# Optimization experiments

Measured on AMD Instinct MI355X. Metric: run time of the kernel, lower is better.

## Reference

```python
import jax, jax.numpy as jnp
import numpy as np
from jax import lax

RF = 19       # receptive field: layers*(kernel-1)+1 = 3*6+1
WINDOW = 12
N_MIX = 2
K = 20        # subgraph_size (top-k per row)
GDEP = 2
ALPHA = 0.05  # propalpha
EPS = 1e-5


def conv2d(x, w, b):
    # x: [N,C,H,W], w: [O,I,1,k], valid conv along time (last) axis
    o = lax.conv_general_dilated(x, w, (1, 1), 'VALID',
                                 dimension_numbers=('NCHW', 'OIHW', 'NCHW'))
    return o + b[None, :, None, None]


def dilated_inception(x, ws, b):
    # ws: kernels [co, ci, k] for k in (2,3,6,7); dilation factor is 1 here
    outs = [lax.conv_general_dilated(x, w[:, :, None, :], (1, 1), 'VALID',
                                     dimension_numbers=('NCHW', 'OIHW', 'NCHW'))
            for w in ws]
    L = outs[-1].shape[-1]  # truncate to shortest (largest kernel) length
    out = jnp.concatenate([o[..., -L:] for o in outs], axis=1)
    return out + b[None, :, None, None]


def build_adj(e1, e2, l1w, l1b, l2w, l2b):
    # e1,e2: [M2,N,D] embedding tables (idx = arange -> full table)
    # torch Linear: y = x @ W.T + b, W: [out,in]
    nv1 = jnp.einsum('mnd,mod->mno', e1, l1w) + l1b[:, None, :]
    nv2 = jnp.einsum('mnd,mod->mno', e2, l2w) + l2b[:, None, :]
    a = jnp.einsum('mnd,mkd->mnk', nv1, nv2)  # [M2, N, N] per-block adjacency
    rows = [jnp.concatenate([a[i * N_MIX + j] for j in range(N_MIX)], axis=1)
            for i in range(N_MIX)]
    adj = jnp.concatenate(rows, axis=0)  # [NT, NT]
    _, t = lax.top_k(adj, K)  # per-row top-k indices
    mask = jnp.zeros_like(adj).at[jnp.arange(adj.shape[0])[:, None], t].set(1.0)
    return adj * mask


def mixprop(x, adj, w, b):
    a = adj + jnp.eye(adj.shape[0], dtype=adj.dtype)
    a = a / jnp.sum(a, axis=1, keepdims=True)  # row-normalize
    h = x
    outs = [h]
    for _ in range(GDEP):
        h = ALPHA * x + (1.0 - ALPHA) * jnp.einsum('ncwl,vw->ncvl', h, a)
        outs.append(h)
    ho = jnp.concatenate(outs, axis=1)  # [B,(GDEP+1)*C,V,L]
    return jnp.einsum('ncvl,oc->novl', ho, w) + b[None, :, None, None]


def layernorm(x, w, b):
    # torch F.layer_norm over all dims except batch; idx = arange -> full affine
    mu = jnp.mean(x, axis=(1, 2, 3), keepdims=True)
    var = jnp.mean((x - mu) ** 2, axis=(1, 2, 3), keepdims=True)
    return (x - mu) * lax.rsqrt(var + EPS) * w[None] + b[None]


def setup_inputs() -> dict:
    keys = iter(jax.random.split(jax.random.key(0), 80))
    def rn(shape, s=0.1):
        return s * jax.random.normal(next(keys), shape, dtype=jnp.float32)
    d = {}
    d['x_in'] = jax.random.normal(next(keys), (32, 12, 500, 4), dtype=jnp.float32)
    d['start_w'] = rn((32, 1, 1, 1)); d['start_b'] = rn((32,))
    d['skip0_w'] = rn((64, 1, 1, 19)); d['skip0_b'] = rn((64,))
    d['emb1'] = rn((3, 4, 500, 40)); d['emb2'] = rn((3, 4, 500, 40))
    d['lin1_w'] = rn((3, 4, 40, 40)); d['lin1_b'] = rn((3, 4, 40))
    d['lin2_w'] = rn((3, 4, 40, 40)); d['lin2_b'] = rn((3, 4, 40))
    d['g1_w'] = rn((3, 32, 96)); d['g1_b'] = rn((3, 32))
    d['g2_w'] = rn((3, 32, 96)); d['g2_b'] = rn((3, 32))
    for pref in ('filt', 'gate'):
        for k in (2, 3, 6, 7):
            d[f'{pref}_w{k}'] = rn((3, 8, 32, k))
        d[f'{pref}_b'] = rn((3, 32))
    for i, L in zip((1, 2, 3), (13, 7, 1)):
        d[f'skip_w{i}'] = rn((64, 32, 1, L)); d[f'skip_b{i}'] = rn((64,))
        d[f'norm_w{i}'] = jnp.ones((32, 1000, L), jnp.float32)
        d[f'norm_b{i}'] = jnp.zeros((32, 1000, L), jnp.float32)
    d['skipE_w'] = rn((64, 32, 1, 1)); d['skipE_b'] = rn((64,))
    d['end1_w'] = rn((128, 64, 1, 1)); d['end1_b'] = rn((128,))
    d['end2_w'] = rn((12, 128, 1, 1)); d['end2_b'] = rn((12,))
    return d


def reference(x_in, start_w, start_b, skip0_w, skip0_b, emb1, emb2,
              lin1_w, lin1_b, lin2_w, lin2_b, g1_w, g1_b, g2_w, g2_b,
              filt_w2, filt_w3, filt_w6, filt_w7, filt_b,
              gate_w2, gate_w3, gate_w6, gate_w7, gate_b,
              skip_w1, skip_b1, skip_w2, skip_b2, skip_w3, skip_b3,
              norm_w1, norm_b1, norm_w2, norm_b2, norm_w3, norm_b3,
              skipE_w, skipE_b, end1_w, end1_b, end2_w, end2_b):
    feat = x_in[..., :-2]  # drop last 2 'time' features
    # split per-mode feature and stack along node dim: [B,T,2N,1]
    inp = jnp.concatenate([feat[..., 0:1], feat[..., 1:2]], axis=2)
    inp = jnp.transpose(inp, (0, 3, 2, 1))  # [B,1,2N,T]
    inp = jnp.pad(inp, ((0, 0), (0, 0), (0, 0), (RF - WINDOW, 0)))
    x = conv2d(inp, start_w, start_b)       # [B,32,1000,19]
    skip = conv2d(inp, skip0_w, skip0_b)    # [B,64,1000,1] (dropout=eval no-op)
    filt_ws = (filt_w2, filt_w3, filt_w6, filt_w7)
    gate_ws = (gate_w2, gate_w3, gate_w6, gate_w7)
    skips = ((skip_w1, skip_b1), (skip_w2, skip_b2), (skip_w3, skip_b3))
    norms = ((norm_w1, norm_b1), (norm_w2, norm_b2), (norm_w3, norm_b3))
    for i in range(3):
        adp = build_adj(emb1[i], emb2[i], lin1_w[i], lin1_b[i], lin2_w[i], lin2_b[i])
        residual = x
        x = mixprop(x, adp, g1_w[i], g1_b[i]) + mixprop(x, adp.T, g2_w[i], g2_b[i])
        f = jnp.tanh(dilated_inception(x, [w[i] for w in filt_ws], filt_b[i]))
        g = jax.nn.sigmoid(dilated_inception(x, [w[i] for w in gate_ws], gate_b[i]))
        x = f * g
        sw, sb = skips[i]
        skip = conv2d(x, sw, sb) + skip
        x = x + residual[..., -x.shape[3]:]
        nw, nb = norms[i]
        x = layernorm(x, nw, nb)
    skip = conv2d(x, skipE_w, skipE_b) + skip
    x = jax.nn.relu(skip)
    x = jax.nn.relu(conv2d(x, end1_w, end1_b))
    return conv2d(x, end2_w, end2_b)  # [B, horizon*out_dim0=12, 1000, 1]
```

## Files before the change

### kernel.cpp

```cpp
#include <hip/hip_runtime.h>
#include <math.h>


#define ALPHA_C 0.05f
#define EPS_C 1e-5f
#define NBC 32
#define CSCT_CAP 140000

__device__ float g_inp[32 * 19 * 1000];
__device__ float g_skip[32 * 64 * 1000];
__device__ __align__(16) float g_nv1[240000];
__device__ __align__(16) float g_nv2[240000];
__device__ __align__(16) int   g_tkcol[60000];
__device__ __align__(16) float g_tkval[60000];
__device__ float g_inv1[3000];
__device__ int   g_colcnt[3000];
__device__ float g_colsum[3000];
__device__ int   g_rp2[3 * 1001 + 1];
__device__ int   g_fill[3000];
__device__ int   g_cscr[60000];
__device__ float g_cscv[60000];
__device__ float g_inv2[3000];
__device__ float g_stats[3 * 64];
__device__ __align__(16) int2 g_pk1T[60000];
__device__ __align__(16) int2 g_cscT[3 * CSCT_CAP];
__device__ int   g_perm[3 * 1024];
__device__ int   g_degT[3 * 1024];
__device__ int   g_iperm[3 * 1000];
__device__ int   g_tOff[3 * 17];
__device__ float g_B0[(size_t)NBC * 32 * 19 * 1000];
__device__ float g_B1[(size_t)NBC * 32 * 19 * 1000];
__device__ float g_B2[(size_t)NBC * 32 * 19 * 1000];
__device__ float g_B3[(size_t)NBC * 32 * 19 * 1000];
__device__ float g_B4[(size_t)NBC * 32 * 19 * 1000];
__device__ float g_B5[(size_t)NBC * 32 * 19 * 1000];

__device__ __forceinline__ float* bufsel(int s)
{
    switch (s) {
        case 0: return g_B0;
        case 1: return g_B1;
        case 2: return g_B2;
        case 3: return g_B3;
        case 4: return g_B4;
        default: return g_B5;
    }
}

__global__ void k_init()
{
    int i = blockIdx.x * 256 + threadIdx.x;
    if (i < 3000) { g_colcnt[i] = 0; g_colsum[i] = 0.f; g_fill[i] = 0; }
    if (i < 192) g_stats[i] = 0.f;
}

__global__ void k_out_zero(float* __restrict__ out, int n)
{
    int i = blockIdx.x * 256 + threadIdx.x;
    if (i < n) out[i] = 0.0f;
}

__global__ void k_marker(float* __restrict__ out, float v)
{
    if (threadIdx.x == 0) out[0] = v;
}


__global__ void k_build_inp(const float* __restrict__ xin)
{
    int i = blockIdx.x * 256 + threadIdx.x;
    if (i >= 32 * 19 * 1000) return;
    int v = i % 1000;
    int t = (i / 1000) % 19;
    int b = i / 19000;
    float val = 0.f;
    if (t >= 7) {
        int tt = t - 7;
        int n = (v < 500) ? v : v - 500;
        int f = (v < 500) ? 0 : 1;
        val = xin[((b * 12 + tt) * 500 + n) * 4 + f];
    }
    g_inp[i] = val;
}

__global__ void k_nv(const float* __restrict__ e1, const float* __restrict__ e2,
                     const float* __restrict__ w1, const float* __restrict__ b1,
                     const float* __restrict__ w2, const float* __restrict__ b2)
{
    int i = blockIdx.x * 256 + threadIdx.x;
    if (i >= 12 * 500 * 40) return;
    int o = i % 40;
    int n = (i / 40) % 500;
    int m = i / (40 * 500);
    const float4* p1 = (const float4*)(e1 + (m * 500 + n) * 40);
    const float4* pw1 = (const float4*)(w1 + (m * 40 + o) * 40);
    const float4* p2 = (const float4*)(e2 + (m * 500 + n) * 40);
    const float4* pw2 = (const float4*)(w2 + (m * 40 + o) * 40);
    float a1 = b1[m * 40 + o], a2 = b2[m * 40 + o];
    for (int d = 0; d < 10; ++d) {
        float4 x1 = p1[d], y1 = pw1[d];
        float4 x2 = p2[d], y2 = pw2[d];
        a1 += x1.x * y1.x; a1 += x1.y * y1.y; a1 += x1.z * y1.z; a1 += x1.w * y1.w;
        a2 += x2.x * y2.x; a2 += x2.y * y2.y; a2 += x2.z * y2.z; a2 += x2.w * y2.w;
    }
    g_nv1[i] = a1;
    g_nv2[i] = a2;
}

__global__ __launch_bounds__(256) void k_adj_topk()
{
    __shared__ float wvv[4];
    __shared__ int wvi[4];
    __shared__ int wci;
    __shared__ int selc[20];
    __shared__ float selv[20];
    int li = blockIdx.x / 1000;
    int r = blockIdx.x % 1000;
    int tid = threadIdx.x;
    int wv = tid >> 6, lane = tid & 63;
    int bi = r / 500, n = r % 500;
    float rv0, rv1, rv2, rv3;
    {
        auto score = [&](int c) -> float {
            if (c >= 1000) return -INFINITY;
            int bj = c / 500, k = c % 500;
            int mg = li * 4 + 2 * bi + bj;
            const float4* a = (const float4*)(g_nv1 + (mg * 500 + n) * 40);
            const float4* b = (const float4*)(g_nv2 + (mg * 500 + k) * 40);
            float acc = 0.f;
#pragma unroll
            for (int d = 0; d < 10; ++d) {
                float4 av = a[d], bv = b[d];
                acc += av.x * bv.x; acc += av.y * bv.y;
                acc += av.z * bv.z; acc += av.w * bv.w;
            }
            return acc;
        };
        rv0 = score(tid);
        rv1 = score(tid + 256);
        rv2 = score(tid + 512);
        rv3 = score(tid + 768);
    }
    for (int sel = 0; sel < 20; ++sel) {
        float bv = rv0;
        int bidx = tid;
        if (rv1 > bv) { bv = rv1; bidx = tid + 256; }
        if (rv2 > bv) { bv = rv2; bidx = tid + 512; }
        if (rv3 > bv) { bv = rv3; bidx = tid + 768; }
#pragma unroll
        for (int m = 1; m < 64; m <<= 1) {
            float ov = __shfl_xor(bv, m);
            int oi = __shfl_xor(bidx, m);
            if (ov > bv || (ov == bv && oi < bidx)) { bv = ov; bidx = oi; }
        }
        if (lane == 0) { wvv[wv] = bv; wvi[wv] = bidx; }
        __syncthreads();
        if (tid == 0) {
            float fv = wvv[0];
            int fi = wvi[0];
#pragma unroll
            for (int k = 1; k < 4; ++k) {
                float ov = wvv[k];
                int oi = wvi[k];
                if (ov > fv || (ov == fv && oi < fi)) { fv = ov; fi = oi; }
            }
            int ci = fi;
            if (ci < 0 || ci > 999) ci = sel;
            selc[sel] = ci;
            selv[sel] = fv;
            g_tkcol[(li * 1000 + r) * 20 + sel] = ci;
            g_tkval[(li * 1000 + r) * 20 + sel] = fv;
            wci = ci;
        }
        __syncthreads();
        int ci = wci;
        if ((ci & 255) == tid) {
            int k = ci >> 8;
            if (k == 0) rv0 = -INFINITY;
            else if (k == 1) rv1 = -INFINITY;
            else if (k == 2) rv2 = -INFINITY;
            else rv3 = -INFINITY;
        }
    }
    if (tid < 20) {
        atomicAdd(&g_colcnt[li * 1000 + selc[tid]], 1);
        atomicAdd(&g_colsum[li * 1000 + selc[tid]], selv[tid]);
    }
    if (tid == 0) {
        float s = 0.f;
        for (int j = 0; j < 20; ++j) s += selv[j];
        g_inv1[li * 1000 + r] = 1.f / (s + 1.f);
    }
}

__global__ __launch_bounds__(256) void k_scan()
{
    __shared__ int s[1000];
    int li = blockIdx.x;
    int tid = threadIdx.x;
    for (int i = tid; i < 1000; i += 256) s[i] = g_colcnt[li * 1000 + i];
    __syncthreads();
    if (tid == 0) {
        int run = 0;
        for (int i = 0; i < 1000; ++i) { int c = s[i]; s[i] = run; run += c; }
        g_rp2[li * 1001 + 1000] = run;
    }
    __syncthreads();
    for (int i = tid; i < 1000; i += 256) {
        g_rp2[li * 1001 + i] = s[i];
        g_inv2[li * 1000 + i] = 1.f / (g_colsum[li * 1000 + i] + 1.f);
    }
}

__global__ __launch_bounds__(256) void k_permsort()
{
    __shared__ int deg[1000];
    __shared__ int tmax[16];
    int li = blockIdx.x;
    int tid = threadIdx.x;
    for (int v = tid; v < 1000; v += 256)
        deg[v] = g_rp2[li * 1001 + v + 1] - g_rp2[li * 1001 + v];
    __syncthreads();
    for (int v = tid; v < 1000; v += 256) {
        int d = deg[v];
        int r = 0;
        for (int u = 0; u < 1000; ++u) {
            int du = deg[u];
            r += (du > d) || (du == d && u < v);
        }
        g_perm[li * 1024 + r] = v;
        g_degT[li * 1024 + r] = d;
        g_iperm[li * 1000 + v] = r;
        if ((r & 63) == 0) tmax[r >> 6] = d;
    }
    if (tid < 24) {
        g_perm[li * 1024 + 1000 + tid] = -1;
        g_degT[li * 1024 + 1000 + tid] = 0;
    }
    __syncthreads();
    if (tid == 0) {
        int off = 0;
        for (int t = 0; t < 16; ++t) {
            g_tOff[li * 17 + t] = off;
            off += 64 * tmax[t];
        }
        g_tOff[li * 17 + 16] = off;
    }
}

__global__ void k_scatter()
{
    int i = blockIdx.x * 256 + threadIdx.x;
    if (i >= 3 * 20000) return;
    int li = i / 20000;
    int e = i % 20000;
    int r = e / 20;
    int c = g_tkcol[i];
    if (c < 0) c = 0;
    if (c > 999) c = 999;
    float v = g_tkval[i];
    int pos = g_rp2[li * 1001 + c] + atomicAdd(&g_fill[li * 1000 + c], 1);
    if (pos < 0) pos = 0;
    if (pos > 19999) pos = 19999;
    g_cscr[li * 20000 + pos] = r;
    g_cscv[li * 20000 + pos] = v;
}

__global__ void k_packT1()
{
    int i = blockIdx.x * 256 + threadIdx.x;
    if (i >= 60000) return;
    int li = i / 20000;
    int e = i % 20000;
    int v = e / 20, j = e % 20;
    int c1 = g_tkcol[i];
    if (c1 < 0) c1 = 0;
    if (c1 > 999) c1 = 999;
    g_pk1T[li * 20000 + j * 1000 + v] = make_int2(c1 * 16, __float_as_int(g_tkval[i]));
}

__global__ void k_packT2()
{
    int i = blockIdx.x * 256 + threadIdx.x;
    if (i >= 3000) return;
    int li = i / 1000, v = i % 1000;
    int r = g_iperm[li * 1000 + v];
    int t = r >> 6, ln = r & 63;
    int j0 = g_rp2[li * 1001 + v];
    int d = g_rp2[li * 1001 + v + 1] - j0;
    int base = g_tOff[li * 17 + t];
    for (int j = 0; j < d; ++j) {
        int row = g_cscr[li * 20000 + j0 + j];
        if (row < 0) row = 0;
        if (row > 999) row = 999;
        int pos = base + j * 64 + ln;
        if (pos >= 0 && pos < CSCT_CAP)
            g_cscT[li * CSCT_CAP + pos] =
                make_int2(row * 16, __float_as_int(g_cscv[li * 20000 + j0 + j]));
    }
}


__global__ __launch_bounds__(256) void k_skip0(const float* __restrict__ w,
                                               const float* __restrict__ bb)
{
    __shared__ float s_inp[19 * 32];
    __shared__ float s_w[64 * 19];
    int b = blockIdx.y;
    int v0 = blockIdx.x * 32;
    int tid = threadIdx.x;
    for (int i = tid; i < 64 * 19; i += 256) s_w[i] = w[i];
    for (int i = tid; i < 19 * 32; i += 256) {
        int t = i / 32, vl = i % 32;
        int v = v0 + vl;
        s_inp[i] = (v < 1000) ? g_inp[(b * 19 + t) * 1000 + v] : 0.f;
    }
    __syncthreads();
    for (int e = tid; e < 64 * 32; e += 256) {
        int o = e / 32, vl = e % 32;
        int v = v0 + vl;
        if (v >= 1000) continue;
        float acc = bb[o];
#pragma unroll
        for (int t = 0; t < 19; ++t) acc += s_w[o * 19 + t] * s_inp[t * 32 + vl];
        g_skip[(b * 64 + o) * 1000 + v] = acc;
    }
}

__global__ __launch_bounds__(256, 5) void k_prop4(int xsel, int o1s, int o2s, int o3s, int o4s,
                                                  int li, int CH, int li0,
                                                  const float* __restrict__ sw,
                                                  const float* __restrict__ sb)
{
    __shared__ float4 S[2000];
    const float* X = bufsel(xsel);
    float* o1 = bufsel(o1s);
    float* o2 = bufsel(o2s);
    float* o3 = bufsel(o3s);
    float* o4 = bufsel(o4s);
    const int2* pkT = g_pk1T + li * 20000;
    const int2* cT = g_cscT + (size_t)li * CSCT_CAP;
    const int* prm = g_perm + li * 1024;
    const int* dgT = g_degT + li * 1024;
    const int* tOf = g_tOff + li * 17;
    const float* iv1 = g_inv1 + li * 1000;
    const float* iv2 = g_inv2 + li * 1000;
    int n = blockIdx.y;
    int ch0 = blockIdx.x * 4;
    size_t gb = ((size_t)n * CH + ch0) * 1000;
    int tid = threadIdx.x;
    int wv = tid >> 6, lane = tid & 63;
    char* Ub = (char*)S;
    char* Wb = (char*)(S + 1000);
    float4* U4 = S;
    float4* W4 = S + 1000;

    auto csr_hop = [&](const char* sbuf, float4* dst, float* gout) {
        for (int it = 0; it < 4; ++it) {
            int v = it * 256 + tid;
            if (v >= 1000) break;
            const int2* mp = pkT + v;
            float4 a = *(const float4*)(sbuf + (size_t)v * 16);
#pragma unroll
            for (int jb = 0; jb < 5; ++jb) {
                int2 e0 = mp[(jb * 4 + 0) * 1000];
                int2 e1 = mp[(jb * 4 + 1) * 1000];
                int2 e2 = mp[(jb * 4 + 2) * 1000];
                int2 e3 = mp[(jb * 4 + 3) * 1000];
                float w0 = __int_as_float(e0.y), w1 = __int_as_float(e1.y);
                float w2 = __int_as_float(e2.y), w3 = __int_as_float(e3.y);
                float4 x0 = *(const float4*)(sbuf + e0.x);
                float4 x1 = *(const float4*)(sbuf + e1.x);
                float4 x2 = *(const float4*)(sbuf + e2.x);
                float4 x3 = *(const float4*)(sbuf + e3.x);
                a.x += w0 * x0.x + w1 * x1.x + w2 * x2.x + w3 * x3.x;
                a.y += w0 * x0.y + w1 * x1.y + w2 * x2.y + w3 * x3.y;
                a.z += w0 * x0.z + w1 * x1.z + w2 * x2.z + w3 * x3.z;
                a.w += w0 * x0.w + w1 * x1.w + w2 * x2.w + w3 * x3.w;
            }
            float s = iv1[v];
            a.x *= s; a.y *= s; a.z *= s; a.w *= s;
            if (dst) dst[v] = a;
            gout[gb + v] = a.x;
            gout[gb + 1000 + v] = a.y;
            gout[gb + 2000 + v] = a.z;
            gout[gb + 3000 + v] = a.w;
        }
    };

    auto csc_hop = [&](const char* sbuf, float4* dst) {
        for (int o = 0; o < 4; ++o) {
            int tile = o * 4 + ((o & 1) ? (3 - wv) : wv);
            int r = tile * 64 + lane;
            int v = prm[r];
            if (v < 0) continue;
            int d = dgT[r];
            const int2* mp = cT + tOf[tile] + lane;
            float4 a = *(const float4*)(sbuf + (size_t)v * 16);
            int j = 0;
            for (; j + 4 <= d; j += 4) {
                int2 e0 = mp[(j + 0) * 64];
                int2 e1 = mp[(j + 1) * 64];
                int2 e2 = mp[(j + 2) * 64];
                int2 e3 = mp[(j + 3) * 64];
                float w0 = __int_as_float(e0.y), w1 = __int_as_float(e1.y);
                float w2 = __int_as_float(e2.y), w3 = __int_as_float(e3.y);
                float4 x0 = *(const float4*)(sbuf + e0.x);
                float4 x1 = *(const float4*)(sbuf + e1.x);
                float4 x2 = *(const float4*)(sbuf + e2.x);
                float4 x3 = *(const float4*)(sbuf + e3.x);
                a.x += w0 * x0.x + w1 * x1.x + w2 * x2.x + w3 * x3.x;
                a.y += w0 * x0.y + w1 * x1.y + w2 * x2.y + w3 * x3.y;
                a.z += w0 * x0.z + w1 * x1.z + w2 * x2.z + w3 * x3.z;
                a.w += w0 * x0.w + w1 * x1.w + w2 * x2.w + w3 * x3.w;
            }
            for (; j < d; ++j) {
                int2 e = mp[j * 64];
                float w = __int_as_float(e.y);
                float4 x = *(const float4*)(sbuf + e.x);
                a.x += w * x.x; a.y += w * x.y; a.z += w * x.z; a.w += w * x.w;
            }
            float s = iv2[v];
            a.x *= s; a.y *= s; a.z *= s; a.w *= s;
            dst[v] = a;
        }
    };

    if (li0) {
        float swv0 = sw[(ch0 + 0) / 19], sbv0 = sb[(ch0 + 0) / 19];
        float swv1 = sw[(ch0 + 1) / 19], sbv1 = sb[(ch0 + 1) / 19];
        float swv2 = sw[(ch0 + 2) / 19], sbv2 = sb[(ch0 + 2) / 19];
        float swv3 = sw[(ch0 + 3) / 19], sbv3 = sb[(ch0 + 3) / 19];
        const float* i0 = g_inp + (n * 19 + (ch0 + 0) % 19) * 1000;
        const float* i1 = g_inp + (n * 19 + (ch0 + 1) % 19) * 1000;
        const float* i2 = g_inp + (n * 19 + (ch0 + 2) % 19) * 1000;
        const float* i3 = g_inp + (n * 19 + (ch0 + 3) % 19) * 1000;
        for (int it = 0; it < 4; ++it) {
            int v = it * 256 + tid;
            if (v >= 1000) break;
            float4 t;
            t.x = swv0 * i0[v] + sbv0;
            t.y = swv1 * i1[v] + sbv1;
            t.z = swv2 * i2[v] + sbv2;
            t.w = swv3 * i3[v] + sbv3;
            U4[v] = t;
        }
    } else {
        for (int it = 0; it < 4; ++it) {
            int v = it * 256 + tid;
            if (v >= 1000) break;
            float4 t;
            t.x = X[gb + v];
            t.y = X[gb + 1000 + v];
            t.z = X[gb + 2000 + v];
            t.w = X[gb + 3000 + v];
            U4[v] = t;
        }
    }
    __syncthreads();

    csr_hop(Ub, W4, o1);
    __syncthreads();

    csr_hop(Wb, (float4*)nullptr, o2);
    __syncthreads();

    csc_hop(Ub, W4);
    __syncthreads();

    for (int it = 0; it < 4; ++it) {
        int v = it * 256 + tid;
        if (v >= 1000) break;
        float4 t = W4[v];
        o3[gb + v] = t.x;
        o3[gb + 1000 + v] = t.y;
        o3[gb + 2000 + v] = t.z;
        o3[gb + 3000 + v] = t.w;
    }
    csc_hop(Wb, U4);
    __syncthreads();

    for (int it = 0; it < 4; ++it) {
        int v = it * 256 + tid;
        if (v >= 1000) break;
        float4 t = U4[v];
        o4[gb + v] = t.x;
        o4[gb + 1000 + v] = t.y;
        o4[gb + 2000 + v] = t.z;
        o4[gb + 3000 + v] = t.w;
    }
}

__global__ __launch_bounds__(256) void k_mix(int xs, int h1s, int h2s, int h3s, int h4s, int ms,
                                             const float* __restrict__ g1w, const float* __restrict__ g2w,
                                             const float* __restrict__ g1b, const float* __restrict__ g2b,
                                             int P, int li0,
                                             const float* __restrict__ sw_,
                                             const float* __restrict__ sb_)
{
    __shared__ float sW[5 * 1024];
    __shared__ float sB[32];
    __shared__ float sWS[32];
    __shared__ float sSB[32];
    int tid = threadIdx.x;
    const float A = ALPHA_C, Bq = 1.f - ALPHA_C;
    for (int i = tid; i < 1024; i += 256) {
        int o = i >> 5, c = i & 31;
        float w1 = g1w[o * 96 + 32 + c], w2 = g1w[o * 96 + 64 + c];
        float w3 = g2w[o * 96 + 32 + c], w4 = g2w[o * 96 + 64 + c];
        sW[i]        = g1w[o * 96 + c] + g2w[o * 96 + c] + A * (w1 + w2 + w3 + w4);
        sW[1024 + i] = Bq * (w1 + A * w2);
        sW[2048 + i] = Bq * Bq * w2;
        sW[3072 + i] = Bq * (w3 + A * w4);
        sW[4096 + i] = Bq * Bq * w4;
    }
    if (tid < 32) sB[tid] = g1b[tid] + g2b[tid];
    __syncthreads();
    if (li0 && tid < 32) {
        float as = 0.f, ab = 0.f;
        for (int c = 0; c < 32; ++c) {
            float w = sW[tid * 32 + c];
            as += w * sw_[c];
            ab += w * sb_[c];
        }
        sWS[tid] = as;
        sSB[tid] = ab;
    }
    if (li0) __syncthreads();
    int n = blockIdx.y;
    int p = blockIdx.x * 256 + tid;
    if (p >= P) return;
    const float* srcs[5] = {bufsel(xs), bufsel(h1s), bufsel(h2s), bufsel(h3s), bufsel(h4s)};
    float acc[32];
    int st0;
    if (li0) {
        float xv = g_inp[(size_t)n * 19000 + p];
#pragma unroll
        for (int o = 0; o < 32; ++o) acc[o] = sB[o] + sSB[o] + sWS[o] * xv;
        st0 = 1;
    } else {
#pragma unroll
        for (int o = 0; o < 32; ++o) acc[o] = sB[o];
        st0 = 0;
    }
    for (int st = st0; st < 5; ++st) {
        const float* src = srcs[st] + (size_t)n * 32 * P + p;
        const float* w = &sW[st * 1024];
        for (int c = 0; c < 32; ++c) {
            float hv = src[(size_t)c * P];
#pragma unroll
            for (int o = 0; o < 32; ++o) acc[o] += w[o * 32 + c] * hv;
        }
    }
    float* XM = bufsel(ms) + (size_t)n * 32 * P + p;
#pragma unroll
    for (int o = 0; o < 32; ++o) XM[(size_t)o * P] = acc[o];
}

template <int LIN>
__global__ __launch_bounds__(256) void k_incept(int xmsel, int xgsel, int xpsel,
                                                const float* __restrict__ fw2, const float* __restrict__ fw3,
                                                const float* __restrict__ fw6, const float* __restrict__ fw7,
                                                const float* __restrict__ fb,
                                                const float* __restrict__ gw2, const float* __restrict__ gw3,
                                                const float* __restrict__ gw6, const float* __restrict__ gw7,
                                                const float* __restrict__ gb,
                                                const float* __restrict__ skw, const float* __restrict__ skb,
                                                int li, int li0,
                                                const float* __restrict__ sw_,
                                                const float* __restrict__ sb_)
{
    const int LOUT = LIN - 6;
    const float* XM = bufsel(xmsel);
    float* XG = bufsel(xgsel);
    const float* Xp = bufsel(xpsel);
    float* stats = g_stats + li * 64;
    __shared__ float sx[32 * 8 * LIN];
    __shared__ float sxg[32 * 8 * LOUT];
    __shared__ float ws1[4], ws2[4];
    int tid = threadIdx.x;
    int n = blockIdx.y, v0 = blockIdx.x * 8;
    for (int i = tid; i < 32 * LIN * 8; i += 256) {
        int vl = i & 7;
        int l = (i >> 3) % LIN;
        int c = i / (8 * LIN);
        sx[(c * 8 + vl) * LIN + l] = XM[(((size_t)n * 32 + c) * LIN + l) * 1000 + v0 + vl];
    }
    __syncthreads();
    int co = tid >> 3, vl = tid & 7;
    int s = co >> 3, co_s = co & 7;
    const int ksz[4] = {2, 3, 6, 7};
    int k = ksz[s];
    const float* fw = (s == 0) ? fw2 : ((s == 1) ? fw3 : ((s == 2) ? fw6 : fw7));
    const float* gw = (s == 0) ? gw2 : ((s == 1) ? gw3 : ((s == 2) ? gw6 : gw7));
    float accf[LOUT], accg[LOUT];
    float bf = fb[co], bg = gb[co];
#pragma unroll
    for (int l = 0; l < LOUT; ++l) { accf[l] = bf; accg[l] = bg; }
    for (int c = 0; c < 32; ++c) {
        const float* xp = &sx[(c * 8 + vl) * LIN];
        for (int j = 0; j < k; ++j) {
            float wf = fw[(co_s * 32 + c) * k + j];
            float wg = gw[(co_s * 32 + c) * k + j];
            int base = 7 - k + j;
#pragma unroll
            for (int l = 0; l < LOUT; ++l) {
                float xv = xp[base + l];
                accf[l] += wf * xv;
                accg[l] += wg * xv;
            }
        }
    }
    size_t ob = ((size_t)n * 32 + co) * LOUT * 1000 + v0 + vl;
    float lsum = 0.f, lss = 0.f;
    float swc = li0 ? sw_[co] : 0.f;
    float sbc = li0 ? sb_[co] : 0.f;
#pragma unroll
    for (int l = 0; l < LOUT; ++l) {
        float g = tanhf(accf[l]) * (1.f / (1.f + expf(-accg[l])));
        float r;
        if (li0)
            r = swc * g_inp[(n * 19 + l + 6) * 1000 + v0 + vl] + sbc;
        else
            r = Xp[(((size_t)n * 32 + co) * LIN + l + 6) * 1000 + v0 + vl];
        float y = g + r;
        XG[ob + (size_t)l * 1000] = y;
        sxg[(co * 8 + vl) * LOUT + l] = g;
        lsum += y;
        lss += y * y;
    }
    __syncthreads();
    int obk = tid >> 3;
    for (int half = 0; half < 2; ++half) {
        int o = obk + 32 * half;
        float acc = skb[o];
        for (int c = 0; c < 32; ++c) {
            const float* wp = &skw[((size_t)o * 32 + c) * LOUT];
            const float* xp = &sxg[(c * 8 + vl) * LOUT];
#pragma unroll
            for (int l = 0; l < LOUT; ++l) acc += wp[l] * xp[l];
        }
        size_t si = ((size_t)n * 64 + o) * 1000 + v0 + vl;
        g_skip[si] += acc;
    }
#pragma unroll
    for (int m = 1; m < 64; m <<= 1) {
        lsum += __shfl_xor(lsum, m);
        lss += __shfl_xor(lss, m);
    }
    int wvi = tid >> 6;
    if ((tid & 63) == 0) { ws1[wvi] = lsum; ws2[wvi] = lss; }
    __syncthreads();
    if (tid == 0) {
        float t1 = ws1[0] + ws1[1] + ws1[2] + ws1[3];
        float t2 = ws2[0] + ws2[1] + ws2[2] + ws2[3];
        atomicAdd(&stats[n * 2], t1);
        atomicAdd(&stats[n * 2 + 1], t2);
    }
}

__global__ void k_norm(int xnsel, const float* __restrict__ nw,
                       const float* __restrict__ nb, int li, int LOUT)
{
    float* XN = bufsel(xnsel);
    const float* stats = g_stats + li * 64;
    int S = 32 * LOUT * 1000;
    long long total = (long long)NBC * S;
    long long stride = (long long)gridDim.x * 256;
    for (long long i = (long long)blockIdx.x * 256 + threadIdx.x; i < total; i += stride) {
        int n = (int)(i / S);
        int rem = (int)(i % S);
        int v = rem % 1000;
        int l = (rem / 1000) % LOUT;
        int c = rem / (1000 * LOUT);
        int widx = (c * 1000 + v) * LOUT + l;
        float cnt = (float)S;
        float mu = stats[n * 2] / cnt;
        float var = stats[n * 2 + 1] / cnt - mu * mu;
        float rs = rsqrtf(var + EPS_C);
        XN[i] = (XN[i] - mu) * rs * nw[widx] + nb[widx];
    }
}

__global__ __launch_bounds__(256) void k_final(int xsel,
                                               const float* __restrict__ ew, const float* __restrict__ eb,
                                               const float* __restrict__ e1w, const float* __restrict__ e1b,
                                               const float* __restrict__ e2w, const float* __restrict__ e2b,
                                               float* __restrict__ out)
{
    const float* X = bufsel(xsel);
    __shared__ float sxf[32 * 16];
    __shared__ float sk[64 * 16];
    __shared__ float s1[64 * 16];
    __shared__ float s2[128 * 16];
    int b = blockIdx.y, v0 = blockIdx.x * 16;
    int tid = threadIdx.x;
    for (int i = tid; i < 512; i += 256) {
        int c = i / 16, vl = i & 15;
        int v = v0 + vl;
        sxf[i] = (v < 1000) ? X[((size_t)b * 32 + c) * 1000 + v] : 0.f;
    }
    for (int i = tid; i < 1024; i += 256) {
        int o = i / 16, vl = i & 15;
        int v = v0 + vl;
        sk[i] = (v < 1000) ? g_skip[((size_t)b * 64 + o) * 1000 + v] : 0.f;
    }
    __syncthreads();
    for (int i = tid; i < 1024; i += 256) {
        int o = i / 16, vl = i & 15;
        float acc = sk[i] + eb[o];
        for (int c = 0; c < 32; ++c) acc += ew[o * 32 + c] * sxf[c * 16 + vl];
        s1[i] = fmaxf(acc, 0.f);
    }
    __syncthreads();
    for (int i = tid; i < 2048; i += 256) {
        int o = i / 16, vl = i & 15;
        float acc = e1b[o];
        for (int c = 0; c < 64; ++c) acc += e1w[o * 64 + c] * s1[c * 16 + vl];
        s2[i] = fmaxf(acc, 0.f);
    }
    __syncthreads();
    if (tid < 192) {
        int o = tid / 16, vl = tid & 15;
        int v = v0 + vl;
        if (v < 1000) {
            float acc = e2b[o];
            for (int c = 0; c < 128; ++c) acc += e2w[o * 128 + c] * s2[c * 16 + vl];
            out[((size_t)b * 12 + o) * 1000 + v] = acc;
        }
    }
}


static const int SZ_SORT[43] = {240000,240000,128,8192,12,1536,96,1536,2304,4608,
                                5376,96,9216,96,9216,96,1536,2304,4608,5376,
                                480,19200,480,19200,416000,224000,32000,416000,224000,32000,
                                64,1216,64,2048,64,64,64,26624,14336,2048,32,32,768000};
static const int SZ_DICT[43] = {768000,32,32,1216,64,240000,240000,19200,480,19200,
                                480,9216,96,9216,96,1536,2304,4608,5376,96,
                                1536,2304,4608,5376,96,26624,64,416000,416000,14336,
                                64,224000,224000,2048,64,32000,32000,2048,64,8192,128,1536,12};
static const int SZ_SIG[43]  = {768000,32,32,1216,64,240000,240000,19200,480,19200,
                                480,9216,96,9216,96,1536,2304,4608,5376,96,
                                1536,2304,4608,5376,96,26624,64,14336,64,2048,
                                64,416000,416000,224000,224000,32000,32000,2048,64,8192,128,1536,12};

extern "C" void kernel_launch(void* const* d_in, const int* in_sizes, int n_in,
                              void* d_out, int out_size, void* d_ws, size_t ws_size,
                              hipStream_t stream)
{
    (void)d_ws; (void)ws_size;
    const float *x_in, *start_w, *start_b, *skip0_w, *skip0_b;
    const float *emb1, *emb2, *lin1_w, *lin1_b, *lin2_w, *lin2_b;
    const float *g1_w, *g1_b, *g2_w, *g2_b;
    const float *filt_w[4], *filt_b, *gate_w[4], *gate_b;
    const float *skw[3], *skb[3], *nww[3], *nbb[3];
    const float *skipE_w, *skipE_b, *end1_w, *end1_b, *end2_w, *end2_b;
    float* outp = (float*)d_out;
    auto P = [&](int i) { return (const float*)d_in[i]; };
    auto match = [&](const int* tab) {
        if (n_in < 43) return false;
        for (int i = 0; i < 43; ++i) if (in_sizes[i] != tab[i]) return false;
        return true;
    };

    int fam = -1;
    if (match(SZ_SORT)) fam = 0;
    else if (match(SZ_DICT)) fam = 1;
    else if (match(SZ_SIG)) fam = 2;

    if (fam == 0) {
        emb1 = P(0); emb2 = P(1); end1_b = P(2); end1_w = P(3); end2_b = P(4); end2_w = P(5);
        filt_b = P(6); filt_w[0] = P(7); filt_w[1] = P(8); filt_w[2] = P(9); filt_w[3] = P(10);
        g1_b = P(11); g1_w = P(12); g2_b = P(13); g2_w = P(14);
        gate_b = P(15); gate_w[0] = P(16); gate_w[1] = P(17); gate_w[2] = P(18); gate_w[3] = P(19);
        lin1_b = P(20); lin1_w = P(21); lin2_b = P(22); lin2_w = P(23);
        nbb[0] = P(24); nbb[1] = P(25); nbb[2] = P(26);
        nww[0] = P(27); nww[1] = P(28); nww[2] = P(29);
        skip0_b = P(30); skip0_w = P(31); skipE_b = P(32); skipE_w = P(33);
        skb[0] = P(34); skb[1] = P(35); skb[2] = P(36);
        skw[0] = P(37); skw[1] = P(38); skw[2] = P(39);
        start_b = P(40); start_w = P(41); x_in = P(42);
    } else if (fam == 1 || fam == 2) {
        x_in = P(0); start_w = P(1); start_b = P(2); skip0_w = P(3); skip0_b = P(4);
        emb1 = P(5); emb2 = P(6); lin1_w = P(7); lin1_b = P(8); lin2_w = P(9); lin2_b = P(10);
        g1_w = P(11); g1_b = P(12); g2_w = P(13); g2_b = P(14);
        filt_w[0] = P(15); filt_w[1] = P(16); filt_w[2] = P(17); filt_w[3] = P(18); filt_b = P(19);
        gate_w[0] = P(20); gate_w[1] = P(21); gate_w[2] = P(22); gate_w[3] = P(23); gate_b = P(24);
        if (fam == 1) {
            skw[0] = P(25); skb[0] = P(26); nww[0] = P(27); nbb[0] = P(28);
            skw[1] = P(29); skb[1] = P(30); nww[1] = P(31); nbb[1] = P(32);
            skw[2] = P(33); skb[2] = P(34); nww[2] = P(35); nbb[2] = P(36);
        } else {
            skw[0] = P(25); skb[0] = P(26); skw[1] = P(27); skb[1] = P(28);
            skw[2] = P(29); skb[2] = P(30);
            nww[0] = P(31); nbb[0] = P(32); nww[1] = P(33); nbb[1] = P(34);
            nww[2] = P(35); nbb[2] = P(36);
        }
        skipE_w = P(37); skipE_b = P(38); end1_w = P(39); end1_b = P(40);
        end2_w = P(41); end2_b = P(42);
    } else {
        k_out_zero<<<(out_size + 255) / 256, 256, 0, stream>>>(outp, out_size);
        k_marker<<<1, 64, 0, stream>>>(outp, 8192.0f);
        return;
    }

    k_init<<<12, 256, 0, stream>>>();
    k_build_inp<<<(32 * 19 * 1000 + 255) / 256, 256, 0, stream>>>(x_in);
    k_nv<<<(240000 + 255) / 256, 256, 0, stream>>>(emb1, emb2, lin1_w, lin1_b, lin2_w, lin2_b);
    k_adj_topk<<<3000, 256, 0, stream>>>();
    k_scan<<<3, 256, 0, stream>>>();
    k_permsort<<<3, 256, 0, stream>>>();
    k_scatter<<<(60000 + 255) / 256, 256, 0, stream>>>();
    k_packT1<<<(60000 + 255) / 256, 256, 0, stream>>>();
    k_packT2<<<12, 256, 0, stream>>>();

    k_skip0<<<dim3(32, NBC), 256, 0, stream>>>(skip0_w, skip0_b);

    int X = 0;
    int LIN = 19;
    for (int li = 0; li < 3; ++li) {
        int LOUT = LIN - 6;
        int Pp = 1000 * LIN;
        int li0 = (li == 0) ? 1 : 0;
        int hb[4], hn = 0;
        for (int b = 0; b < 6 && hn < 4; ++b)
            if (b != X && b != 1) hb[hn++] = b;
        int h1 = hb[0], h2 = hb[1], h3 = hb[2], h4 = hb[3];
        int CH = 32 * LIN;
        dim3 gg((unsigned)(CH / 4), NBC);

        k_prop4<<<gg, 256, 0, stream>>>(X, h1, h2, h3, h4, li, CH, li0, start_w, start_b);

        k_mix<<<dim3((Pp + 255) / 256, NBC), 256, 0, stream>>>(X, h1, h2, h3, h4, 1,
            g1_w + li * 3072, g2_w + li * 3072, g1_b + li * 32, g2_b + li * 32, Pp,
            li0, start_w, start_b);

        int XG = h1;
        if (LIN == 19)
            k_incept<19><<<dim3(125, NBC), 256, 0, stream>>>(1, XG, X,
                filt_w[0] + li * 512, filt_w[1] + li * 768, filt_w[2] + li * 1536, filt_w[3] + li * 1792,
                filt_b + li * 32,
                gate_w[0] + li * 512, gate_w[1] + li * 768, gate_w[2] + li * 1536, gate_w[3] + li * 1792,
                gate_b + li * 32, skw[li], skb[li], li, li0, start_w, start_b);
        else if (LIN == 13)
            k_incept<13><<<dim3(125, NBC), 256, 0, stream>>>(1, XG, X,
                filt_w[0] + li * 512, filt_w[1] + li * 768, filt_w[2] + li * 1536, filt_w[3] + li * 1792,
                filt_b + li * 32,
                gate_w[0] + li * 512, gate_w[1] + li * 768, gate_w[2] + li * 1536, gate_w[3] + li * 1792,
                gate_b + li * 32, skw[li], skb[li], li, li0, start_w, start_b);
        else
            k_incept<7><<<dim3(125, NBC), 256, 0, stream>>>(1, XG, X,
                filt_w[0] + li * 512, filt_w[1] + li * 768, filt_w[2] + li * 1536, filt_w[3] + li * 1792,
                filt_b + li * 32,
                gate_w[0] + li * 512, gate_w[1] + li * 768, gate_w[2] + li * 1536, gate_w[3] + li * 1792,
                gate_b + li * 32, skw[li], skb[li], li, li0, start_w, start_b);

        k_norm<<<2048, 256, 0, stream>>>(XG, nww[li], nbb[li], li, LOUT);

        X = XG;
        LIN = LOUT;
    }
    k_final<<<dim3(63, NBC), 256, 0, stream>>>(X, skipE_w, skipE_b,
                                               end1_w, end1_b, end2_w, end2_b, outp);
}
```

Before: 2.581 ms.

## Fuse layernorm into downstream consumer kernels and drop standalone norm pass

Removes the separate k_norm kernel that rewrote each layer's output in place. The normalization (using precomputed per-sample stats and affine weights) is applied on the fly wherever the un-normalized activation is read: in the propagation kernel, the mix kernel's first stage, the inception residual path, and the final kernel. This saves a full read/write pass over the activation per layer, but adds strided gathers of the affine weights and redundant normalization work in several consumers.

```diff
diff --git a/kernel.cpp b/kernel.cpp
--- a/kernel.cpp
+++ b/kernel.cpp
@@ -330,7 +330,9 @@
 __global__ __launch_bounds__(256, 5) void k_prop4(int xsel, int o1s, int o2s, int o3s, int o4s,
                                                   int li, int CH, int li0,
                                                   const float* __restrict__ sw,
-                                                  const float* __restrict__ sb)
+                                                  const float* __restrict__ sb,
+                                                  const float* __restrict__ nwp,
+                                                  const float* __restrict__ nbp)
 {
     __shared__ float4 S[2000];
     const float* X = bufsel(xsel);
@@ -446,14 +448,32 @@
             U4[v] = t;
         }
     } else {
+        int L = CH >> 5;
+        const float* pst = g_stats + (li - 1) * 64;
+        float cnt = 32.f * (float)L * 1000.f;
+        float mu = pst[n * 2] / cnt;
+        float var = pst[n * 2 + 1] / cnt - mu * mu;
+        float rs = rsqrtf(var + EPS_C);
+        int c0 = (ch0 + 0) / L, l0 = (ch0 + 0) % L;
+        int c1 = (ch0 + 1) / L, l1 = (ch0 + 1) % L;
+        int c2 = (ch0 + 2) / L, l2 = (ch0 + 2) % L;
+        int c3 = (ch0 + 3) / L, l3 = (ch0 + 3) % L;
+        const float* nw0 = nwp + c0 * 1000 * L + l0;
+        const float* nw1 = nwp + c1 * 1000 * L + l1;
+        const float* nw2 = nwp + c2 * 1000 * L + l2;
+        const float* nw3 = nwp + c3 * 1000 * L + l3;
+        const float* nb0 = nbp + c0 * 1000 * L + l0;
+        const float* nb1 = nbp + c1 * 1000 * L + l1;
+        const float* nb2 = nbp + c2 * 1000 * L + l2;
+        const float* nb3 = nbp + c3 * 1000 * L + l3;
         for (int it = 0; it < 4; ++it) {
             int v = it * 256 + tid;
             if (v >= 1000) break;
             float4 t;
-            t.x = X[gb + v];
-            t.y = X[gb + 1000 + v];
-            t.z = X[gb + 2000 + v];
-            t.w = X[gb + 3000 + v];
+            t.x = (X[gb + v] - mu) * rs * nw0[v * L] + nb0[v * L];
+            t.y = (X[gb + 1000 + v] - mu) * rs * nw1[v * L] + nb1[v * L];
+            t.z = (X[gb + 2000 + v] - mu) * rs * nw2[v * L] + nb2[v * L];
+            t.w = (X[gb + 3000 + v] - mu) * rs * nw3[v * L] + nb3[v * L];
             U4[v] = t;
         }
     }
@@ -494,9 +514,11 @@
 __global__ __launch_bounds__(256) void k_mix(int xs, int h1s, int h2s, int h3s, int h4s, int ms,
                                              const float* __restrict__ g1w, const float* __restrict__ g2w,
                                              const float* __restrict__ g1b, const float* __restrict__ g2b,
-                                             int P, int li0,
+                                             int P, int li, int li0,
                                              const float* __restrict__ sw_,
-                                             const float* __restrict__ sb_)
+                                             const float* __restrict__ sb_,
+                                             const float* __restrict__ nwp,
+                                             const float* __restrict__ nbp)
 {
     __shared__ float sW[5 * 1024];
     __shared__ float sB[32];
@@ -532,18 +554,30 @@
     if (p >= P) return;
     const float* srcs[5] = {bufsel(xs), bufsel(h1s), bufsel(h2s), bufsel(h3s), bufsel(h4s)};
     float acc[32];
-    int st0;
     if (li0) {
         float xv = g_inp[(size_t)n * 19000 + p];
 #pragma unroll
         for (int o = 0; o < 32; ++o) acc[o] = sB[o] + sSB[o] + sWS[o] * xv;
-        st0 = 1;
     } else {
 #pragma unroll
         for (int o = 0; o < 32; ++o) acc[o] = sB[o];
-        st0 = 0;
-    }
-    for (int st = st0; st < 5; ++st) {
+        int L = P / 1000;
+        int l = p / 1000, v = p - l * 1000;
+        const float* pst = g_stats + (li - 1) * 64;
+        float cnt = 32.f * (float)P;
+        float mu = pst[n * 2] / cnt;
+        float var = pst[n * 2 + 1] / cnt - mu * mu;
+        float rs = rsqrtf(var + EPS_C);
+        const float* src0 = srcs[0] + (size_t)n * 32 * P + p;
+        int wbase = v * L + l;
+        for (int c = 0; c < 32; ++c) {
+            int wi = c * 1000 * L + wbase;
+            float hv = (src0[(size_t)c * P] - mu) * rs * nwp[wi] + nbp[wi];
+#pragma unroll
+            for (int o = 0; o < 32; ++o) acc[o] += sW[o * 32 + c] * hv;
+        }
+    }
+    for (int st = 1; st < 5; ++st) {
         const float* src = srcs[st] + (size_t)n * 32 * P + p;
         const float* w = &sW[st * 1024];
         for (int c = 0; c < 32; ++c) {
@@ -568,7 +602,9 @@
                                                 const float* __restrict__ skw, const float* __restrict__ skb,
                                                 int li, int li0,
                                                 const float* __restrict__ sw_,
-                                                const float* __restrict__ sb_)
+                                                const float* __restrict__ sb_,
+                                                const float* __restrict__ nwp,
+                                                const float* __restrict__ nbp)
 {
     const int LOUT = LIN - 6;
     const float* XM = bufsel(xmsel);
@@ -615,14 +651,25 @@
     float lsum = 0.f, lss = 0.f;
     float swc = li0 ? sw_[co] : 0.f;
     float sbc = li0 ? sb_[co] : 0.f;
+    float mu = 0.f, rs = 0.f;
+    if (!li0) {
+        const float* pst = g_stats + (li - 1) * 64;
+        float cnt = 32.f * (float)LIN * 1000.f;
+        mu = pst[n * 2] / cnt;
+        float var = pst[n * 2 + 1] / cnt - mu * mu;
+        rs = rsqrtf(var + EPS_C);
+    }
 #pragma unroll
     for (int l = 0; l < LOUT; ++l) {
         float g = tanhf(accf[l]) * (1.f / (1.f + expf(-accg[l])));
         float r;
-        if (li0)
+        if (li0) {
             r = swc * g_inp[(n * 19 + l + 6) * 1000 + v0 + vl] + sbc;
-        else
-            r = Xp[(((size_t)n * 32 + co) * LIN + l + 6) * 1000 + v0 + vl];
+        } else {
+            float raw = Xp[(((size_t)n * 32 + co) * LIN + l + 6) * 1000 + v0 + vl];
+            int wi = (co * 1000 + v0 + vl) * LIN + l + 6;
+            r = (raw - mu) * rs * nwp[wi] + nbp[wi];
+        }
         float y = g + r;
         XG[ob + (size_t)l * 1000] = y;
         sxg[(co * 8 + vl) * LOUT + l] = g;
@@ -659,33 +706,11 @@
     }
 }
 
-__global__ void k_norm(int xnsel, const float* __restrict__ nw,
-                       const float* __restrict__ nb, int li, int LOUT)
-{
-    float* XN = bufsel(xnsel);
-    const float* stats = g_stats + li * 64;
-    int S = 32 * LOUT * 1000;
-    long long total = (long long)NBC * S;
-    long long stride = (long long)gridDim.x * 256;
-    for (long long i = (long long)blockIdx.x * 256 + threadIdx.x; i < total; i += stride) {
-        int n = (int)(i / S);
-        int rem = (int)(i % S);
-        int v = rem % 1000;
-        int l = (rem / 1000) % LOUT;
-        int c = rem / (1000 * LOUT);
-        int widx = (c * 1000 + v) * LOUT + l;
-        float cnt = (float)S;
-        float mu = stats[n * 2] / cnt;
-        float var = stats[n * 2 + 1] / cnt - mu * mu;
-        float rs = rsqrtf(var + EPS_C);
-        XN[i] = (XN[i] - mu) * rs * nw[widx] + nb[widx];
-    }
-}
-
 __global__ __launch_bounds__(256) void k_final(int xsel,
                                                const float* __restrict__ ew, const float* __restrict__ eb,
                                                const float* __restrict__ e1w, const float* __restrict__ e1b,
                                                const float* __restrict__ e2w, const float* __restrict__ e2b,
+                                               const float* __restrict__ nw2, const float* __restrict__ nb2,
                                                float* __restrict__ out)
 {
     const float* X = bufsel(xsel);
@@ -695,10 +720,21 @@
     __shared__ float s2[128 * 16];
     int b = blockIdx.y, v0 = blockIdx.x * 16;
     int tid = threadIdx.x;
+    const float* pst = g_stats + 2 * 64;
+    float cnt = 32000.f;
+    float mu = pst[b * 2] / cnt;
+    float var = pst[b * 2 + 1] / cnt - mu * mu;
+    float rs = rsqrtf(var + EPS_C);
     for (int i = tid; i < 512; i += 256) {
         int c = i / 16, vl = i & 15;
         int v = v0 + vl;
-        sxf[i] = (v < 1000) ? X[((size_t)b * 32 + c) * 1000 + v] : 0.f;
+        float x = 0.f;
+        if (v < 1000) {
+            float raw = X[((size_t)b * 32 + c) * 1000 + v];
+            int wi = c * 1000 + v;
+            x = (raw - mu) * rs * nw2[wi] + nb2[wi];
+        }
+        sxf[i] = x;
     }
     for (int i = tid; i < 1024; i += 256) {
         int o = i / 16, vl = i & 15;
@@ -823,6 +859,8 @@
         int LOUT = LIN - 6;
         int Pp = 1000 * LIN;
         int li0 = (li == 0) ? 1 : 0;
+        const float* nwp = li0 ? start_w : nww[li - 1];
+        const float* nbp = li0 ? start_b : nbb[li - 1];
         int hb[4], hn = 0;
         for (int b = 0; b < 6 && hn < 4; ++b)
             if (b != X && b != 1) hb[hn++] = b;
@@ -830,11 +868,12 @@
         int CH = 32 * LIN;
         dim3 gg((unsigned)(CH / 4), NBC);
 
-        k_prop4<<<gg, 256, 0, stream>>>(X, h1, h2, h3, h4, li, CH, li0, start_w, start_b);
+        k_prop4<<<gg, 256, 0, stream>>>(X, h1, h2, h3, h4, li, CH, li0,
+                                        start_w, start_b, nwp, nbp);
 
         k_mix<<<dim3((Pp + 255) / 256, NBC), 256, 0, stream>>>(X, h1, h2, h3, h4, 1,
             g1_w + li * 3072, g2_w + li * 3072, g1_b + li * 32, g2_b + li * 32, Pp,
-            li0, start_w, start_b);
+            li, li0, start_w, start_b, nwp, nbp);
 
         int XG = h1;
         if (LIN == 19)
@@ -842,25 +881,24 @@
                 filt_w[0] + li * 512, filt_w[1] + li * 768, filt_w[2] + li * 1536, filt_w[3] + li * 1792,
                 filt_b + li * 32,
                 gate_w[0] + li * 512, gate_w[1] + li * 768, gate_w[2] + li * 1536, gate_w[3] + li * 1792,
-                gate_b + li * 32, skw[li], skb[li], li, li0, start_w, start_b);
+                gate_b + li * 32, skw[li], skb[li], li, li0, start_w, start_b, nwp, nbp);
         else if (LIN == 13)
             k_incept<13><<<dim3(125, NBC), 256, 0, stream>>>(1, XG, X,
                 filt_w[0] + li * 512, filt_w[1] + li * 768, filt_w[2] + li * 1536, filt_w[3] + li * 1792,
                 filt_b + li * 32,
                 gate_w[0] + li * 512, gate_w[1] + li * 768, gate_w[2] + li * 1536, gate_w[3] + li * 1792,
-                gate_b + li * 32, skw[li], skb[li], li, li0, start_w, start_b);
+                gate_b + li * 32, skw[li], skb[li], li, li0, start_w, start_b, nwp, nbp);
         else
             k_incept<7><<<dim3(125, NBC), 256, 0, stream>>>(1, XG, X,
                 filt_w[0] + li * 512, filt_w[1] + li * 768, filt_w[2] + li * 1536, filt_w[3] + li * 1792,
                 filt_b + li * 32,
                 gate_w[0] + li * 512, gate_w[1] + li * 768, gate_w[2] + li * 1536, gate_w[3] + li * 1792,
-                gate_b + li * 32, skw[li], skb[li], li, li0, start_w, start_b);
-
-        k_norm<<<2048, 256, 0, stream>>>(XG, nww[li], nbb[li], li, LOUT);
+                gate_b + li * 32, skw[li], skb[li], li, li0, start_w, start_b, nwp, nbp);
 
         X = XG;
         LIN = LOUT;
     }
     k_final<<<dim3(63, NBC), 256, 0, stream>>>(X, skipE_w, skipE_b,
-                                               end1_w, end1_b, end2_w, end2_b, outp);
-}
+                                               end1_w, end1_b, end2_w, end2_b,
+                                               nww[2], nbb[2], outp);
+}
```

Result: no change. 2.571 ms (-0.4%).
